# Performance work log

Hardware: AMD Instinct MI355X
Metric: run time of the kernel (lower is better)

The kernel has to match this reference:

```python
import jax, jax.numpy as jnp
import numpy as np

N_POOL = 500_000   # number of source neurons (value store size)
N_W = 1024         # number of unique (deduplicated) weight matrices
E = 1_000_000      # number of connections (neuron-input pairs)
D_IN = 16
D_OUT = 16


def setup_inputs() -> dict:
    key = jax.random.key(0)
    k1, k2, k3, k4 = jax.random.split(key, 4)
    values = jax.random.normal(k1, (N_POOL, D_IN), dtype=jnp.float32)
    weight = jax.random.normal(k2, (N_W, D_OUT, D_IN), dtype=jnp.float32)
    input_idx = jax.random.randint(k3, (E,), 0, N_POOL, dtype=jnp.int64) if jax.config.jax_enable_x64 else jax.random.randint(k3, (E,), 0, N_POOL).astype(jnp.int32)
    weight_idx = jax.random.randint(k4, (E,), 0, N_W).astype(jnp.int32)
    return {"values": values, "weight": weight, "input_idx": input_idx, "weight_idx": weight_idx}


def reference(values, weight, input_idx, weight_idx):
    # LINEAR_GATHER: gather input value vectors per connection  -> [E, D_IN]
    x = values[input_idx]
    # LINEAR_WEIGHTS_GATHER: gather weight matrices per connection -> [E, D_OUT, D_IN]
    w = weight[weight_idx]
    # LINEAR_LINEAR: per-connection matmul (w @ input_values) -> [E, D_OUT]
    y = jnp.einsum('eoi,ei->eo', w, x)
    return y
```

## Files before the change

kernel.cpp:

```cpp
#include <hip/hip_runtime.h>
#include <hip/hip_fp16.h>


#define D 16
#define WPB 4
#define TPB (WPB * 64)
#define MAXBLK 2048

typedef _Float16 h2v __attribute__((ext_vector_type(2)));

__global__ __launch_bounds__(256) void linear_gather_mv(
    const float* __restrict__ values, const float* __restrict__ weight,
    const int* __restrict__ input_idx, const int* __restrict__ weight_idx,
    float* __restrict__ out, int E)
{
    int tid = blockIdx.x * blockDim.x + threadIdx.x;
    int e = tid >> 2;
    int j = tid & 3;
    if (e >= E) return;
    int ii = input_idx[e];
    int wi = weight_idx[e];
    const float4* xp = (const float4*)(values + (long long)ii * D);
    float4 x0 = xp[0], x1 = xp[1], x2 = xp[2], x3 = xp[3];
    const float4* wp = (const float4*)(weight + (long long)wi * (D * D) + j * (4 * D));
    float4 acc;
    float* accp = (float*)&acc;
    #pragma unroll
    for (int r = 0; r < 4; ++r) {
        float4 w0 = wp[r * 4 + 0], w1 = wp[r * 4 + 1], w2 = wp[r * 4 + 2], w3 = wp[r * 4 + 3];
        accp[r] = w0.x * x0.x + w0.y * x0.y + w0.z * x0.z + w0.w * x0.w
                + w1.x * x1.x + w1.y * x1.y + w1.z * x1.z + w1.w * x1.w
                + w2.x * x2.x + w2.y * x2.y + w2.z * x2.z + w2.w * x2.w
                + w3.x * x3.x + w3.y * x3.y + w3.z * x3.z + w3.w * x3.w;
    }
    ((float4*)out)[(long long)e * 4 + j] = acc;
}

__global__ __launch_bounds__(256) void wconv(
    const float* __restrict__ w, __half* __restrict__ wh, int n)
{
    int i = (blockIdx.x * 256 + threadIdx.x) * 4;
    if (i + 3 >= n) {
        for (int k = i; k < n; ++k) wh[k] = __float2half(w[k]);
        return;
    }
    float4 v = *(const float4*)(w + i);
    __half2 a = __floats2half2_rn(v.x, v.y);
    __half2 b = __floats2half2_rn(v.z, v.w);
    float2 packed;
    ((__half2*)&packed)[0] = a;
    ((__half2*)&packed)[1] = b;
    *(float2*)(wh + i) = packed;
}

#define WPAIR(K, W0, W1) do {                                                  \
    int a0 = __builtin_amdgcn_readlane(wcur, 4*(K)+0);                         \
    int a1 = __builtin_amdgcn_readlane(wcur, 4*(K)+1);                         \
    int a2 = __builtin_amdgcn_readlane(wcur, 4*(K)+2);                         \
    int a3 = __builtin_amdgcn_readlane(wcur, 4*(K)+3);                         \
    W0 = ((const float4*)(wh + (long long)(lh ? a1 : a0) * (D*D)))[hrow];      \
    W1 = ((const float4*)(wh + (long long)(lh ? a3 : a2) * (D*D)))[hrow];      \
} while (0)

#define STEP(CC, WV, YS) do {                                                  \
    int c  = (CC) + lh;                                                        \
    float4 xv = *(const float4*)(xh + (size_t)c * D + (h << 3));               \
    const h2v* xp2 = (const h2v*)&xv;                                          \
    const h2v* wp2 = (const h2v*)&(WV);                                        \
    float p = __builtin_amdgcn_fdot2(wp2[0], xp2[0], 0.0f, false);             \
    p = __builtin_amdgcn_fdot2(wp2[1], xp2[1], p, false);                      \
    p = __builtin_amdgcn_fdot2(wp2[2], xp2[2], p, false);                      \
    p = __builtin_amdgcn_fdot2(wp2[3], xp2[3], p, false);                      \
    p += __shfl_xor(p, 1);            \
    YS = p;                                                                    \
} while (0)

#define COMP4(K, W0, W1) do {                                                  \
    float ys0, ys1;                                                            \
    STEP(4*(K)+0, W0, ys0);                                                    \
    STEP(4*(K)+2, W1, ys1);                                                    \
    float v0 = __shfl(ys0, srcl);                                              \
    float v1 = __shfl(ys1, srcl);                                              \
    float yv = (lane & 2) ? v1 : v0;                                           \
    int cc = 4*(K) + (lane & 3);                                               \
    if (cc < nb) outb[(long long)cc * D + pr] = yv;                            \
} while (0)

#define GATHER(BI) do {                                                        \
    int kl = (BI) * 64 + lane; if (kl >= E) kl = E - 1;                        \
    iv    = iidx[kl];                                                          \
    wnext = widx[kl];                                                          \
    int iiu;                                                                   \
    iiu = __shfl(iv,      g4); xq0 = ((const float4*)(values + (long long)iiu * D))[q]; \
    iiu = __shfl(iv, 16 + g4); xq1 = ((const float4*)(values + (long long)iiu * D))[q]; \
    iiu = __shfl(iv, 32 + g4); xq2 = ((const float4*)(values + (long long)iiu * D))[q]; \
    iiu = __shfl(iv, 48 + g4); xq3 = ((const float4*)(values + (long long)iiu * D))[q]; \
} while (0)

#define COMMIT(U, XQ) do {                                                     \
    __half2 c0 = __floats2half2_rn((XQ).x, (XQ).y);                            \
    __half2 c1 = __floats2half2_rn((XQ).z, (XQ).w);                            \
    float2 pk;                                                                 \
    ((__half2*)&pk)[0] = c0;                                                   \
    ((__half2*)&pk)[1] = c1;                                                   \
    *(float2*)(xh + ((U)*16 + g4) * D + (q << 2)) = pk;                        \
} while (0)

__global__ __launch_bounds__(TPB, 4) void direct_mv(
    const float* __restrict__ values, const __half* __restrict__ wh,
    const int* __restrict__ iidx, const int* __restrict__ widx,
    float* __restrict__ out, int E)
{
    __shared__ _Float16 xh_all[WPB * 64 * D];
    const int lane = threadIdx.x & 63;
    const int wid  = threadIdx.x >> 6;
    _Float16* xh = xh_all + wid * (64 * D);
    const int g4 = lane >> 2;
    const int q  = lane & 3;
    const int lh   = lane >> 5;
    const int h    = lane & 1;
    const int hrow = lane & 31;
    const int pr   = lane >> 2;
    const int srcl = 32 * (lane & 1) + 2 * (lane >> 2);

    const int nbatch = (E + 63) >> 6;
    const int gw = blockIdx.x * WPB + wid;
    const int GW = gridDim.x * WPB;
    if (gw >= nbatch) return;

    int iv, wnext;
    float4 xq0, xq1, xq2, xq3;
    GATHER(gw);

    for (int bi = gw; bi < nbatch; bi += GW) {
        COMMIT(0, xq0);
        COMMIT(1, xq1);
        COMMIT(2, xq2);
        COMMIT(3, xq3);
        int wcur = wnext;
        int k0 = bi * 64;
        int nb = E - k0; if (nb > 64) nb = 64;
        float* outb = out + (long long)k0 * D;

        int bn = bi + GW;
        if (bn < nbatch) GATHER(bn);

        float4 P0, P1, Q0, Q1;
        WPAIR( 0, P0, P1);
        WPAIR( 1, Q0, Q1);
        COMP4( 0, P0, P1); WPAIR( 2, P0, P1);
        COMP4( 1, Q0, Q1); WPAIR( 3, Q0, Q1);
        COMP4( 2, P0, P1); WPAIR( 4, P0, P1);
        COMP4( 3, Q0, Q1); WPAIR( 5, Q0, Q1);
        COMP4( 4, P0, P1); WPAIR( 6, P0, P1);
        COMP4( 5, Q0, Q1); WPAIR( 7, Q0, Q1);
        COMP4( 6, P0, P1); WPAIR( 8, P0, P1);
        COMP4( 7, Q0, Q1); WPAIR( 9, Q0, Q1);
        COMP4( 8, P0, P1); WPAIR(10, P0, P1);
        COMP4( 9, Q0, Q1); WPAIR(11, Q0, Q1);
        COMP4(10, P0, P1); WPAIR(12, P0, P1);
        COMP4(11, Q0, Q1); WPAIR(13, Q0, Q1);
        COMP4(12, P0, P1); WPAIR(14, P0, P1);
        COMP4(13, Q0, Q1); WPAIR(15, Q0, Q1);
        COMP4(14, P0, P1);
        COMP4(15, Q0, Q1);
    }
}

extern "C" void kernel_launch(void* const* d_in, const int* in_sizes, int n_in,
                              void* d_out, int out_size, void* d_ws, size_t ws_size,
                              hipStream_t stream) {
    const float* values     = (const float*)d_in[0];
    const float* weight     = (const float*)d_in[1];
    const int*   input_idx  = (const int*)d_in[2];
    const int*   weight_idx = (const int*)d_in[3];
    float*       out        = (float*)d_out;

    int E = in_sizes[2];
    if (E <= 0) return;
    int NW = in_sizes[1] / (D * D);
    size_t need = (size_t)NW * D * D * sizeof(__half);

    if (ws_size < need) {
        int total_thr = E * 4;
        int grid = (total_thr + 255) / 256;
        hipLaunchKernelGGL(linear_gather_mv, dim3(grid), dim3(256), 0, stream,
                           values, weight, input_idx, weight_idx, out, E);
        return;
    }

    __half* wh = (__half*)d_ws;
    int nconv = NW * D * D;
    int cblk = (nconv / 4 + 255) / 256;
    hipLaunchKernelGGL(wconv, dim3(cblk), dim3(256), 0, stream,
                       weight, wh, nconv);

    int nbatch = (E + 63) >> 6;
    int nblk = (nbatch + WPB - 1) / WPB;
    if (nblk > MAXBLK) nblk = MAXBLK;
    hipLaunchKernelGGL(direct_mv, dim3(nblk), dim3(TPB), 0, stream,
                       values, wh, input_idx, weight_idx, out, E);
}
```

Before: 130.7 us.

## Stage outputs through LDS for vectorized stores and prefetch indices two batches ahead

Each lane now writes its reduced dot product as fp16 into a per-wave LDS buffer. The wave then reads it back and emits float4 global stores covering contiguous 1 KB chunks, replacing the cross-lane shuffles and scalar 4-byte scattered stores. Index loads are split from value gathers and issued two batches ahead, so the value gather for the next batch no longer waits on its index load. Rounding the output to fp16 before widening back to float adds precision loss, and the extra LDS round trip adds latency per batch.

```diff
diff --git a/kernel.cpp b/kernel.cpp
--- a/kernel.cpp
+++ b/kernel.cpp
@@ -62,7 +62,7 @@
     W1 = ((const float4*)(wh + (long long)(lh ? a3 : a2) * (D*D)))[hrow];      \
 } while (0)
 
-#define STEP(CC, WV, YS) do {                                                  \
+#define STEP(CC, WV) do {                                                      \
     int c  = (CC) + lh;                                                        \
     float4 xv = *(const float4*)(xh + (size_t)c * D + (h << 3));               \
     const h2v* xp2 = (const h2v*)&xv;                                          \
@@ -72,29 +72,23 @@
     p = __builtin_amdgcn_fdot2(wp2[2], xp2[2], p, false);                      \
     p = __builtin_amdgcn_fdot2(wp2[3], xp2[3], p, false);                      \
     p += __shfl_xor(p, 1);            \
-    YS = p;                                                                    \
-} while (0)
-
-#define COMP4(K, W0, W1) do {                                                  \
-    float ys0, ys1;                                                            \
-    STEP(4*(K)+0, W0, ys0);                                                    \
-    STEP(4*(K)+2, W1, ys1);                                                    \
-    float v0 = __shfl(ys0, srcl);                                              \
-    float v1 = __shfl(ys1, srcl);                                              \
-    float yv = (lane & 2) ? v1 : v0;                                           \
-    int cc = 4*(K) + (lane & 3);                                               \
-    if (cc < nb) outb[(long long)cc * D + pr] = yv;                            \
-} while (0)
-
-#define GATHER(BI) do {                                                        \
+    if (h == 0) yh[c * D + rr] = (_Float16)p;                                  \
+} while (0)
+
+#define COMP4(K, W0, W1) do { STEP(4*(K)+0, W0); STEP(4*(K)+2, W1); } while (0)
+
+#define IDXLOAD(BI, IV, WV) do {                                               \
     int kl = (BI) * 64 + lane; if (kl >= E) kl = E - 1;                        \
-    iv    = iidx[kl];                                                          \
-    wnext = widx[kl];                                                          \
+    IV = iidx[kl];                                                             \
+    WV = widx[kl];                                                             \
+} while (0)
+
+#define XLOAD(IV) do {                                                         \
     int iiu;                                                                   \
-    iiu = __shfl(iv,      g4); xq0 = ((const float4*)(values + (long long)iiu * D))[q]; \
-    iiu = __shfl(iv, 16 + g4); xq1 = ((const float4*)(values + (long long)iiu * D))[q]; \
-    iiu = __shfl(iv, 32 + g4); xq2 = ((const float4*)(values + (long long)iiu * D))[q]; \
-    iiu = __shfl(iv, 48 + g4); xq3 = ((const float4*)(values + (long long)iiu * D))[q]; \
+    iiu = __shfl(IV,      g4); xq0 = ((const float4*)(values + (long long)iiu * D))[q]; \
+    iiu = __shfl(IV, 16 + g4); xq1 = ((const float4*)(values + (long long)iiu * D))[q]; \
+    iiu = __shfl(IV, 32 + g4); xq2 = ((const float4*)(values + (long long)iiu * D))[q]; \
+    iiu = __shfl(IV, 48 + g4); xq3 = ((const float4*)(values + (long long)iiu * D))[q]; \
 } while (0)
 
 #define COMMIT(U, XQ) do {                                                     \
@@ -112,38 +106,44 @@
     float* __restrict__ out, int E)
 {
     __shared__ _Float16 xh_all[WPB * 64 * D];
+    __shared__ _Float16 yh_all[WPB * 64 * D];
     const int lane = threadIdx.x & 63;
     const int wid  = threadIdx.x >> 6;
     _Float16* xh = xh_all + wid * (64 * D);
+    _Float16* yh = yh_all + wid * (64 * D);
     const int g4 = lane >> 2;
     const int q  = lane & 3;
     const int lh   = lane >> 5;
     const int h    = lane & 1;
     const int hrow = lane & 31;
-    const int pr   = lane >> 2;
-    const int srcl = 32 * (lane & 1) + 2 * (lane >> 2);
+    const int rr   = (lane & 31) >> 1;
 
     const int nbatch = (E + 63) >> 6;
     const int gw = blockIdx.x * WPB + wid;
     const int GW = gridDim.x * WPB;
     if (gw >= nbatch) return;
 
-    int iv, wnext;
+    int ivC, wvC, ivN, wvN;
     float4 xq0, xq1, xq2, xq3;
-    GATHER(gw);
+    IDXLOAD(gw, ivC, wvC);
+    XLOAD(ivC);
+    if (gw + GW < nbatch) IDXLOAD(gw + GW, ivN, wvN);
+    else { ivN = ivC; wvN = wvC; }
 
     for (int bi = gw; bi < nbatch; bi += GW) {
         COMMIT(0, xq0);
         COMMIT(1, xq1);
         COMMIT(2, xq2);
         COMMIT(3, xq3);
-        int wcur = wnext;
+        int wcur = wvC;
         int k0 = bi * 64;
         int nb = E - k0; if (nb > 64) nb = 64;
         float* outb = out + (long long)k0 * D;
 
         int bn = bi + GW;
-        if (bn < nbatch) GATHER(bn);
+        if (bn < nbatch) XLOAD(ivN);
+        int bn2 = bi + 2 * GW;
+        if (bn2 < nbatch) IDXLOAD(bn2, ivC, wvC);
 
         float4 P0, P1, Q0, Q1;
         WPAIR( 0, P0, P1);
@@ -164,6 +164,22 @@
         COMP4(13, Q0, Q1); WPAIR(15, Q0, Q1);
         COMP4(14, P0, P1);
         COMP4(15, Q0, Q1);
+
+        #pragma unroll
+        for (int j = 0; j < 4; ++j) {
+            float2 raw = *(const float2*)((const char*)yh + j * 512 + lane * 8);
+            float2 f0 = __half22float2(((const __half2*)&raw)[0]);
+            float2 f1 = __half22float2(((const __half2*)&raw)[1]);
+            float4 o;
+            o.x = f0.x; o.y = f0.y; o.z = f1.x; o.w = f1.y;
+            int cc = j * 16 + (lane >> 2);
+            if (cc < nb)
+                *(float4*)(outb + (size_t)j * 256 + lane * 4) = o;
+        }
+
+        int t;
+        t = ivC; ivC = ivN; ivN = t;
+        t = wvC; wvC = wvN; wvN = t;
     }
 }
 
```

Measured after the change: 124.5 us. 4.8% less time.
